# Kernel tuning notes

Measured on AMD Instinct MI355X. Metric: run time of the kernel, lower is better.

Reference implementation:

```python
import jax, jax.numpy as jnp
import numpy as np

N_NODES = 32768
N_EDGES = 524288
HID = 128


def _linear_params(key, fan_in, fan_out):
    kw, kb = jax.random.split(key)
    bound = 1.0 / np.sqrt(fan_in)
    w = jax.random.uniform(kw, (fan_in, fan_out), jnp.float32, -bound, bound)
    b = jax.random.uniform(kb, (fan_out,), jnp.float32, -bound, bound)
    return w, b


def setup_inputs() -> dict:
    key = jax.random.key(0)
    ks = jax.random.split(key, 8)
    x = jax.random.normal(ks[0], (N_NODES, HID), jnp.float32)
    edge_attr = jax.random.normal(ks[1], (N_EDGES, HID), jnp.float32)
    edges = jax.random.randint(ks[2], (2, N_EDGES), 0, N_NODES, jnp.int32)
    w1, b1 = _linear_params(ks[3], 3 * HID, HID)      # message_fn layer 1
    w2, b2 = _linear_params(ks[4], HID, HID)          # message_fn layer 2
    wu1, bu1 = _linear_params(ks[5], HID, 2 * HID)    # update_fn layer 1
    wu2, bu2 = _linear_params(ks[6], 2 * HID, HID)    # update_fn layer 2
    return {"x": x, "edge_attr": edge_attr, "edges": edges,
            "w1": w1, "b1": b1, "w2": w2, "b2": b2,
            "wu1": wu1, "bu1": bu1, "wu2": wu2, "bu2": bu2}


def reference(x, edge_attr, edges, w1, b1, w2, b2, wu1, bu1, wu2, bu2):
    n_nodes = x.shape[0]
    send, recv = edges[0], edges[1]
    # gather endpoint features and concat with edge attributes: [E, 3*HID]
    ea = jnp.concatenate([x[send], x[recv], edge_attr], axis=-1)
    # per-edge message MLP (Linear-SiLU-Linear-SiLU)
    h = jax.nn.silu(ea @ w1 + b1)
    msg = jax.nn.silu(h @ w2 + b2)                    # [E, HID]
    # scatter-mean into receiving nodes
    sums = jax.ops.segment_sum(msg, recv, num_segments=n_nodes)
    counts = jax.ops.segment_sum(jnp.ones((msg.shape[0],), msg.dtype), recv,
                                 num_segments=n_nodes)
    aggr = sums / jnp.maximum(counts, 1.0)[:, None]
    # residual (input_size == hidden_size -> Identity) + update MLP
    xo = x + aggr
    xo = xo + (jax.nn.silu(xo @ wu1 + bu1) @ wu2 + bu2)
    return xo, msg
```

## Files before the change

kernel.cpp:

```cpp
#include <hip/hip_runtime.h>
#include <hip/hip_bf16.h>

#define NN 32768
#define NE 524288
#define HID 128

typedef unsigned short u16;
typedef unsigned int u32;
typedef __bf16 bf16x8 __attribute__((ext_vector_type(8)));
typedef float f32x4 __attribute__((ext_vector_type(4)));

__device__ __forceinline__ u16 f2bf(float f) {
  return __builtin_bit_cast(u16, (__bf16)f);
}
__device__ __forceinline__ float silu_f(float v) {
  return v * __builtin_amdgcn_rcpf(1.f + __expf(-v));
}
__device__ __forceinline__ bf16x8 cvt8(float4 a, float4 b) {
  bf16x8 r;
  r[0] = (__bf16)a.x; r[1] = (__bf16)a.y; r[2] = (__bf16)a.z; r[3] = (__bf16)a.w;
  r[4] = (__bf16)b.x; r[5] = (__bf16)b.y; r[6] = (__bf16)b.z; r[7] = (__bf16)b.w;
  return r;
}
__device__ __forceinline__ float4 f4fma(float4 x, float4 s, float inv) {
  return make_float4(x.x + s.x * inv, x.y + s.y * inv,
                     x.z + s.z * inv, x.w + s.w * inv);
}

__device__ __forceinline__ void gld16(const void* g, void* l) {
  __builtin_amdgcn_global_load_lds(
      (const __attribute__((address_space(1))) u32*)g,
      (__attribute__((address_space(3))) u32*)l, 16, 0, 0);
}

#define WV(N)  do { asm volatile("s_waitcnt vmcnt(" #N ")" ::: "memory"); \
                    __builtin_amdgcn_sched_barrier(0); } while (0)
#define WL()   do { asm volatile("s_waitcnt lgkmcnt(0)" ::: "memory"); \
                    __builtin_amdgcn_sched_barrier(0); } while (0)
__device__ __forceinline__ void bar() {
  __builtin_amdgcn_sched_barrier(0);
  __builtin_amdgcn_s_barrier();
  __builtin_amdgcn_sched_barrier(0);
}

__global__ __launch_bounds__(256) void prep_k(
    const float* __restrict__ x, const float* __restrict__ w1,
    const float* __restrict__ w2, const float* __restrict__ wu1,
    const float* __restrict__ wu2, const int* __restrict__ recv,
    u16* __restrict__ xb, u16* __restrict__ w1Ts, u16* __restrict__ w2Ts,
    u16* __restrict__ wu1T, u16* __restrict__ wu2T, int* __restrict__ cnt)
{
  int i = blockIdx.x * 256 + threadIdx.x;
  xb[i] = f2bf(x[i]);
  if (i < NE) atomicAdd(&cnt[recv[i]], 1);
  if (i < 3 * 128 * 128) {
    int j = i & 7, qs = (i >> 3) & 15, c = (i >> 7) & 127, s = i >> 14;
    int k = s * 128 + ((qs ^ (c & 7)) << 3) + j;
    w1Ts[i] = f2bf(w1[k * 128 + c]);
  }
  if (i < 128 * 128) {
    int j = i & 7, qs = (i >> 3) & 15, c = i >> 7;
    int k = ((qs ^ (c & 7)) << 3) + j;
    w2Ts[i] = f2bf(w2[k * 128 + c]);
  }
  if (i < 256 * 128) { int c = i >> 7, k = i & 127; wu1T[i] = f2bf(wu1[k * 256 + c]); }
  if (i < 128 * 256) { int c = i >> 8, k = i & 255; wu2T[i] = f2bf(wu2[k * 128 + c]); }
}

__global__ __launch_bounds__(1024) void scan_k(const int* __restrict__ cnt,
                                               int* __restrict__ cursor)
{
  __shared__ int part[1024];
  const int tid = threadIdx.x;
  const int base = tid * 32;
  int v[32];
  int s = 0;
  #pragma unroll
  for (int j = 0; j < 32; ++j) { v[j] = cnt[base + j]; s += v[j]; }
  part[tid] = s;
  __syncthreads();
  #pragma unroll 1
  for (int d = 1; d < 1024; d <<= 1) {
    int t = (tid >= d) ? part[tid - d] : 0;
    __syncthreads();
    part[tid] += t;
    __syncthreads();
  }
  int ex = part[tid] - s;
  #pragma unroll
  for (int j = 0; j < 32; ++j) {
    cursor[base + j] = ex;
    ex += v[j];
  }
}

__global__ __launch_bounds__(256) void scatter_k(const int* __restrict__ recv,
                                                 int* __restrict__ cursor,
                                                 int* __restrict__ eperm)
{
  int e = blockIdx.x * 256 + threadIdx.x;
  int r = recv[e];
  int pos = atomicAdd(&cursor[r], 1);
  eperm[pos] = e;
}

__global__ __launch_bounds__(512, 4) void edge_mlp(
    const u16* __restrict__ xb, const float* __restrict__ eattr,
    const int* __restrict__ send, const int* __restrict__ recv,
    const int* __restrict__ eperm,
    const u16* __restrict__ w1Ts, const float* __restrict__ b1,
    const u16* __restrict__ w2Ts, const float* __restrict__ b2,
    float* __restrict__ msg_out, float* __restrict__ sums)
{
  __shared__ u16 sA0[64 * 128];
  __shared__ u16 sA1[64 * 128];
  __shared__ u16 sB[128 * 128 / 2 * 2];
  __shared__ int sNid[64];

  const int tid  = threadIdx.x;
  const int lane = tid & 63;
  const int w    = tid >> 6;
  const int wr   = w >> 2;
  const int wc   = w & 3;
  const int fr   = lane & 15;
  const int fkq  = lane >> 4;
  const int orow = fkq * 4;
  const int lrow4 = lane >> 4;
  const int schk  = lane & 15;
  const int logical = ((int)blockIdx.x & 7) * ((int)gridDim.x >> 3)
                    + ((int)blockIdx.x >> 3);
  const int e0 = logical * 64;

  int eo[2], ns[2], nr[2], rl[2];
  #pragma unroll
  for (int i = 0; i < 2; ++i) {
    rl[i] = w * 8 + i * 4 + lrow4;
    eo[i] = eperm[e0 + rl[i]];
  }
  #pragma unroll
  for (int i = 0; i < 2; ++i) {
    ns[i] = send[eo[i]];
    nr[i] = recv[eo[i]];
    if (schk == 0) sNid[rl[i]] = nr[i];
  }

  f32x4 acc[2][2];
  #pragma unroll
  for (int m = 0; m < 2; ++m)
    #pragma unroll
    for (int n = 0; n < 2; ++n)
      #pragma unroll
      for (int r = 0; r < 4; ++r) acc[m][n][r] = 0.f;

  float b1v[2], b2v[2];
  #pragma unroll
  for (int n = 0; n < 2; ++n) {
    b1v[n] = b1[wc * 32 + n * 16 + fr];
    b2v[n] = b2[wc * 32 + n * 16 + fr];
  }
  __builtin_amdgcn_sched_barrier(0);
  #pragma unroll
  for (int i = 0; i < 2; ++i)
    gld16(xb + ((size_t)ns[i] << 7) + ((schk ^ (rl[i] & 7)) << 3),
          sA0 + ((w * 8 + i * 4) << 7));
  #pragma unroll
  for (int i = 0; i < 4; ++i)
    gld16(w1Ts + ((w * 16 + i * 4) << 7) + (lane << 3),
          sB + ((w * 16 + i * 4) << 7));
  __builtin_amdgcn_sched_barrier(0);
  #pragma unroll
  for (int i = 0; i < 2; ++i)
    gld16(xb + ((size_t)nr[i] << 7) + ((schk ^ (rl[i] & 7)) << 3),
          sA1 + ((w * 8 + i * 4) << 7));
  __builtin_amdgcn_sched_barrier(0);
  float4 ea[2][2];
  #pragma unroll
  for (int i = 0; i < 2; ++i) {
    const float* ep = eattr + ((size_t)eo[i] << 7) + ((schk ^ (rl[i] & 7)) << 3);
    ea[i][0] = *reinterpret_cast<const float4*>(ep);
    ea[i][1] = *reinterpret_cast<const float4*>(ep + 4);
  }
  __builtin_amdgcn_sched_barrier(0);

  auto cslice = [&](const u16* bufA) {
    #pragma unroll
    for (int kk = 0; kk < 4; ++kk) {
      bf16x8 aF[2], bF[2];
      #pragma unroll
      for (int m = 0; m < 2; ++m) {
        int row = wr * 32 + m * 16 + fr;
        int ch = (kk * 4 + fkq) ^ (row & 7);
        aF[m] = __builtin_bit_cast(bf16x8,
            *reinterpret_cast<const uint4*>(bufA + (row << 7) + (ch << 3)));
      }
      #pragma unroll
      for (int n = 0; n < 2; ++n) {
        int c = wc * 32 + n * 16 + fr;
        int ch = (kk * 4 + fkq) ^ (c & 7);
        bF[n] = __builtin_bit_cast(bf16x8,
            *reinterpret_cast<const uint4*>(sB + (c << 7) + (ch << 3)));
      }
      __builtin_amdgcn_s_setprio(1);
      #pragma unroll
      for (int m = 0; m < 2; ++m)
        #pragma unroll
        for (int n = 0; n < 2; ++n)
          acc[m][n] = __builtin_amdgcn_mfma_f32_16x16x32_bf16(aF[m], bF[n], acc[m][n], 0, 0, 0);
      __builtin_amdgcn_s_setprio(0);
    }
  };

  WV(6); bar();
  cslice(sA0);
  bar();
  #pragma unroll
  for (int i = 0; i < 4; ++i)
    gld16(w1Ts + 16384 + ((w * 16 + i * 4) << 7) + (lane << 3),
          sB + ((w * 16 + i * 4) << 7));
  WV(0); bar();
  cslice(sA1);
  bar();
  #pragma unroll
  for (int i = 0; i < 2; ++i)
    *reinterpret_cast<uint4*>(sA0 + (rl[i] << 7) + (schk << 3)) =
        __builtin_bit_cast(uint4, cvt8(ea[i][0], ea[i][1]));
  #pragma unroll
  for (int i = 0; i < 4; ++i)
    gld16(w1Ts + 32768 + ((w * 16 + i * 4) << 7) + (lane << 3),
          sB + ((w * 16 + i * 4) << 7));
  WV(0); WL(); bar();
  cslice(sA0);
  bar();
  #pragma unroll
  for (int i = 0; i < 4; ++i)
    gld16(w2Ts + ((w * 16 + i * 4) << 7) + (lane << 3),
          sB + ((w * 16 + i * 4) << 7));
  #pragma unroll
  for (int m = 0; m < 2; ++m)
    #pragma unroll
    for (int n = 0; n < 2; ++n) {
      int c = wc * 32 + n * 16 + fr;
      #pragma unroll
      for (int r = 0; r < 4; ++r) {
        int row = wr * 32 + m * 16 + orow + r;
        sA1[(row << 7) + (((c >> 3) ^ (row & 7)) << 3) + (c & 7)] =
            f2bf(silu_f(acc[m][n][r] + b1v[n]));
        acc[m][n][r] = 0.f;
      }
    }
  WV(0); WL(); bar();
  int eg[2][4];
  #pragma unroll
  for (int m = 0; m < 2; ++m)
    #pragma unroll
    for (int r = 0; r < 4; ++r)
      eg[m][r] = eperm[e0 + wr * 32 + m * 16 + orow + r];
  cslice(sA1);
  bar();

  #pragma unroll
  for (int m = 0; m < 2; ++m)
    #pragma unroll
    for (int r = 0; r < 4; ++r) {
      int row = wr * 32 + m * 16 + orow + r;
      float* mp = msg_out + ((size_t)eg[m][r] << 7);
      #pragma unroll
      for (int n = 0; n < 2; ++n) {
        int c = wc * 32 + n * 16 + fr;
        float v = silu_f(acc[m][n][r] + b2v[n]);
        mp[c] = v;
        sA0[(row << 7) + (((c >> 3) ^ (row & 7)) << 3) + (c & 7)] = f2bf(v);
      }
    }
  WL(); bar();

  {
    const int col = tid & 127, q = tid >> 7;
    float s = 0.f;
    int cur = sNid[q * 16];
    #pragma unroll 1
    for (int r = 0; r < 16; ++r) {
      int row = q * 16 + r;
      u16 hv = sA0[(row << 7) + (((col >> 3) ^ (row & 7)) << 3) + (col & 7)];
      s += __builtin_bit_cast(float, (u32)hv << 16);
      int nxt = (r < 15) ? sNid[row + 1] : -1;
      if (nxt != cur) {
        atomicAdd(sums + (size_t)cur * HID + col, s);
        s = 0.f;
        cur = nxt;
      }
    }
  }
}

__global__ __launch_bounds__(256) void mlp1_k(
    const float* __restrict__ x, const float* __restrict__ sums,
    const int* __restrict__ cnt, const u16* __restrict__ wu1T,
    const float* __restrict__ bu1, u16* __restrict__ t)
{
  __shared__ u16 sB[256][40];
  const int tid = threadIdx.x, lane = tid & 63, wid = tid >> 6;
  const int wr = wid >> 1, wc = wid & 1;
  const int fr = lane & 15, fkq = lane >> 4, fk = fkq * 8, orow = fkq * 4;
  const int n0 = blockIdx.x * 64;

  float invm[2];
  #pragma unroll
  for (int m = 0; m < 2; ++m)
    invm[m] = __builtin_amdgcn_rcpf(fmaxf((float)cnt[n0 + wr * 32 + m * 16 + fr], 1.f));

  f32x4 acc[2][8];
  #pragma unroll
  for (int m = 0; m < 2; ++m)
    #pragma unroll
    for (int n = 0; n < 8; ++n)
      #pragma unroll
      for (int r = 0; r < 4; ++r) acc[m][n][r] = 0.f;

  #pragma unroll 1
  for (int kk = 0; kk < 4; ++kk) {
    #pragma unroll
    for (int it = 0; it < 4; ++it) {
      int chunk = tid + it * 256;
      int c = chunk >> 2, q = chunk & 3;
      *reinterpret_cast<uint4*>(&sB[c][q * 8]) =
          *reinterpret_cast<const uint4*>(wu1T + c * 128 + kk * 32 + q * 8);
    }
    __syncthreads();
    bf16x8 aF[2], bF[8];
    #pragma unroll
    for (int m = 0; m < 2; ++m) {
      size_t base = (size_t)(n0 + wr * 32 + m * 16 + fr) * HID + kk * 32 + fk;
      float4 xv0 = *reinterpret_cast<const float4*>(x + base);
      float4 xv1 = *reinterpret_cast<const float4*>(x + base + 4);
      float4 sv0 = *reinterpret_cast<const float4*>(sums + base);
      float4 sv1 = *reinterpret_cast<const float4*>(sums + base + 4);
      aF[m] = cvt8(f4fma(xv0, sv0, invm[m]), f4fma(xv1, sv1, invm[m]));
    }
    #pragma unroll
    for (int n = 0; n < 8; ++n)
      bF[n] = __builtin_bit_cast(bf16x8,
          *reinterpret_cast<const uint4*>(&sB[wc * 128 + n * 16 + fr][fk]));
    #pragma unroll
    for (int m = 0; m < 2; ++m)
      #pragma unroll
      for (int n = 0; n < 8; ++n)
        acc[m][n] = __builtin_amdgcn_mfma_f32_16x16x32_bf16(aF[m], bF[n], acc[m][n], 0, 0, 0);
    __syncthreads();
  }
  #pragma unroll
  for (int n = 0; n < 8; ++n) {
    int col = wc * 128 + n * 16 + fr;
    float bb = bu1[col];
    #pragma unroll
    for (int m = 0; m < 2; ++m) {
      int row = n0 + wr * 32 + m * 16 + orow;
      #pragma unroll
      for (int r = 0; r < 4; ++r)
        t[(size_t)(row + r) * 256 + col] = f2bf(silu_f(acc[m][n][r] + bb));
    }
  }
}

__global__ __launch_bounds__(256) void mlp2_k(
    const u16* __restrict__ t, const u16* __restrict__ wu2T,
    const float* __restrict__ bu2, const float* __restrict__ x,
    const float* __restrict__ sums, const int* __restrict__ cnt,
    float* __restrict__ xo)
{
  __shared__ u16 sB[128][40];
  const int tid = threadIdx.x, lane = tid & 63, wid = tid >> 6;
  const int wr = wid >> 1, wc = wid & 1;
  const int fr = lane & 15, fk = (lane >> 4) * 8, orow = (lane >> 4) * 4;
  const int n0 = blockIdx.x * 64;

  f32x4 acc[2][4];
  #pragma unroll
  for (int m = 0; m < 2; ++m)
    #pragma unroll
    for (int n = 0; n < 4; ++n)
      #pragma unroll
      for (int r = 0; r < 4; ++r) acc[m][n][r] = 0.f;

  #pragma unroll 1
  for (int kk = 0; kk < 8; ++kk) {
    #pragma unroll
    for (int it = 0; it < 2; ++it) {
      int chunk = tid + it * 256;
      int c = chunk >> 2, q = chunk & 3;
      *reinterpret_cast<uint4*>(&sB[c][q * 8]) =
          *reinterpret_cast<const uint4*>(wu2T + c * 256 + kk * 32 + q * 8);
    }
    __syncthreads();
    bf16x8 aF[2], bF[4];
    #pragma unroll
    for (int m = 0; m < 2; ++m)
      aF[m] = __builtin_bit_cast(bf16x8, *reinterpret_cast<const uint4*>(
          t + (size_t)(n0 + wr * 32 + m * 16 + fr) * 256 + kk * 32 + fk));
    #pragma unroll
    for (int n = 0; n < 4; ++n)
      bF[n] = __builtin_bit_cast(bf16x8,
          *reinterpret_cast<const uint4*>(&sB[wc * 64 + n * 16 + fr][fk]));
    #pragma unroll
    for (int m = 0; m < 2; ++m)
      #pragma unroll
      for (int n = 0; n < 4; ++n)
        acc[m][n] = __builtin_amdgcn_mfma_f32_16x16x32_bf16(aF[m], bF[n], acc[m][n], 0, 0, 0);
    __syncthreads();
  }
  #pragma unroll
  for (int m = 0; m < 2; ++m) {
    #pragma unroll
    for (int r = 0; r < 4; ++r) {
      int gn = n0 + wr * 32 + m * 16 + orow + r;
      float inv = 1.f / fmaxf((float)cnt[gn], 1.f);
      #pragma unroll
      for (int n = 0; n < 4; ++n) {
        int col = wc * 64 + n * 16 + fr;
        float xi = x[(size_t)gn * HID + col] + sums[(size_t)gn * HID + col] * inv;
        xo[(size_t)gn * HID + col] = xi + acc[m][n][r] + bu2[col];
      }
    }
  }
}

extern "C" void kernel_launch(void* const* d_in, const int* in_sizes, int n_in,
                              void* d_out, int out_size, void* d_ws, size_t ws_size,
                              hipStream_t stream)
{
  (void)in_sizes; (void)n_in; (void)out_size; (void)ws_size;
  const float* x     = (const float*)d_in[0];
  const float* eattr = (const float*)d_in[1];
  const int*   edges = (const int*)d_in[2];
  const float* w1  = (const float*)d_in[3];
  const float* b1  = (const float*)d_in[4];
  const float* w2  = (const float*)d_in[5];
  const float* b2  = (const float*)d_in[6];
  const float* wu1 = (const float*)d_in[7];
  const float* bu1 = (const float*)d_in[8];
  const float* wu2 = (const float*)d_in[9];
  const float* bu2 = (const float*)d_in[10];

  float* xo  = (float*)d_out;
  float* msg = xo + (size_t)NN * HID;

  char* p = (char*)d_ws;
  u16* xb    = (u16*)p; p += (size_t)NN * HID * 2;
  u16* w1Ts  = (u16*)p; p += 384 * 128 * 2;
  u16* w2Ts  = (u16*)p; p += 128 * 128 * 2;
  u16* wu1T  = (u16*)p; p += 256 * 128 * 2;
  u16* wu2T  = (u16*)p; p += 128 * 256 * 2;
  u16* tbuf  = (u16*)p; p += (size_t)NN * 256 * 2;
  float* sums = (float*)p; p += (size_t)NN * HID * 4;
  int* cnt    = (int*)p; p += (size_t)NN * 4;
  int* cursor = (int*)p; p += (size_t)NN * 4;
  int* eperm  = (int*)p; p += (size_t)NE * 4;

  const int* send = edges;
  const int* recv = edges + NE;

  hipMemsetAsync(cnt, 0, (size_t)NN * 4, stream);
  hipMemsetAsync(sums, 0, (size_t)NN * HID * 4, stream);
  prep_k<<<NN * HID / 256, 256, 0, stream>>>(x, w1, w2, wu1, wu2, recv,
                                             xb, w1Ts, w2Ts, wu1T, wu2T, cnt);
  scan_k<<<1, 1024, 0, stream>>>(cnt, cursor);
  scatter_k<<<NE / 256, 256, 0, stream>>>(recv, cursor, eperm);
  edge_mlp<<<NE / 64, 512, 0, stream>>>(xb, eattr, send, recv, eperm,
                                        w1Ts, b1, w2Ts, b2, msg, sums);
  mlp1_k<<<NN / 64, 256, 0, stream>>>(x, sums, cnt, wu1T, bu1, tbuf);
  mlp2_k<<<NN / 64, 256, 0, stream>>>(tbuf, wu2T, bu2, x, sums, cnt, xo);
}
```

Before: 327.1 us.

## Make edge MLP persistent with LDS-resident weights and per-wave edge tiles

Rewrites the edge MLP as a persistent kernel of 256 blocks. Each block loads all layer-1 and layer-2 weights into LDS once, then each wave independently processes eight 32-edge tiles. The wave prefetches the next tile's gathered node features into registers and uses a small per-wave LDS scratch for the hidden activations and the segment reduction. The scatter pass now also writes permuted sender/receiver ids, so the MLP avoids indirect index lookups. This removes repeated weight streaming and block-wide barriers, but keeps only one 512-thread block per CU and puts heavy pressure on registers.

```diff
diff --git a/kernel.cpp b/kernel.cpp
--- a/kernel.cpp
+++ b/kernel.cpp
@@ -12,6 +12,9 @@
 
 __device__ __forceinline__ u16 f2bf(float f) {
   return __builtin_bit_cast(u16, (__bf16)f);
+}
+__device__ __forceinline__ float bf2f(u16 h) {
+  return __builtin_bit_cast(float, (u32)h << 16);
 }
 __device__ __forceinline__ float silu_f(float v) {
   return v * __builtin_amdgcn_rcpf(1.f + __expf(-v));
@@ -33,15 +36,8 @@
       (__attribute__((address_space(3))) u32*)l, 16, 0, 0);
 }
 
-#define WV(N)  do { asm volatile("s_waitcnt vmcnt(" #N ")" ::: "memory"); \
-                    __builtin_amdgcn_sched_barrier(0); } while (0)
 #define WL()   do { asm volatile("s_waitcnt lgkmcnt(0)" ::: "memory"); \
                     __builtin_amdgcn_sched_barrier(0); } while (0)
-__device__ __forceinline__ void bar() {
-  __builtin_amdgcn_sched_barrier(0);
-  __builtin_amdgcn_s_barrier();
-  __builtin_amdgcn_sched_barrier(0);
-}
 
 __global__ __launch_bounds__(256) void prep_k(
     const float* __restrict__ x, const float* __restrict__ w1,
@@ -94,202 +90,223 @@
   }
 }
 
-__global__ __launch_bounds__(256) void scatter_k(const int* __restrict__ recv,
+__global__ __launch_bounds__(256) void scatter_k(const int* __restrict__ send,
+                                                 const int* __restrict__ recv,
                                                  int* __restrict__ cursor,
-                                                 int* __restrict__ eperm)
+                                                 int* __restrict__ eperm,
+                                                 int* __restrict__ sid,
+                                                 int* __restrict__ rid)
 {
   int e = blockIdx.x * 256 + threadIdx.x;
   int r = recv[e];
+  int s = send[e];
   int pos = atomicAdd(&cursor[r], 1);
   eperm[pos] = e;
-}
-
-__global__ __launch_bounds__(512, 4) void edge_mlp(
+  sid[pos] = s;
+  rid[pos] = r;
+}
+
+__global__ __launch_bounds__(512, 2) void edge_mlp(
     const u16* __restrict__ xb, const float* __restrict__ eattr,
-    const int* __restrict__ send, const int* __restrict__ recv,
-    const int* __restrict__ eperm,
-    const u16* __restrict__ w1Ts, const float* __restrict__ b1,
-    const u16* __restrict__ w2Ts, const float* __restrict__ b2,
+    const int* __restrict__ eperm, const int* __restrict__ sid,
+    const int* __restrict__ rid,
+    const u16* __restrict__ wTs, const float* __restrict__ b1,
+    const float* __restrict__ b2,
     float* __restrict__ msg_out, float* __restrict__ sums)
 {
-  __shared__ u16 sA0[64 * 128];
-  __shared__ u16 sA1[64 * 128];
-  __shared__ u16 sB[128 * 128 / 2 * 2];
-  __shared__ int sNid[64];
+  __shared__ u16 sW[65536];
+  __shared__ u16 sT[8][1280];
 
   const int tid  = threadIdx.x;
   const int lane = tid & 63;
   const int w    = tid >> 6;
-  const int wr   = w >> 2;
-  const int wc   = w & 3;
   const int fr   = lane & 15;
   const int fkq  = lane >> 4;
   const int orow = fkq * 4;
-  const int lrow4 = lane >> 4;
-  const int schk  = lane & 15;
-  const int logical = ((int)blockIdx.x & 7) * ((int)gridDim.x >> 3)
-                    + ((int)blockIdx.x >> 3);
-  const int e0 = logical * 64;
-
-  int eo[2], ns[2], nr[2], rl[2];
-  #pragma unroll
-  for (int i = 0; i < 2; ++i) {
-    rl[i] = w * 8 + i * 4 + lrow4;
-    eo[i] = eperm[e0 + rl[i]];
-  }
-  #pragma unroll
-  for (int i = 0; i < 2; ++i) {
-    ns[i] = send[eo[i]];
-    nr[i] = recv[eo[i]];
-    if (schk == 0) sNid[rl[i]] = nr[i];
-  }
-
-  f32x4 acc[2][2];
-  #pragma unroll
-  for (int m = 0; m < 2; ++m)
-    #pragma unroll
-    for (int n = 0; n < 2; ++n)
-      #pragma unroll
-      for (int r = 0; r < 4; ++r) acc[m][n][r] = 0.f;
-
-  float b1v[2], b2v[2];
-  #pragma unroll
-  for (int n = 0; n < 2; ++n) {
-    b1v[n] = b1[wc * 32 + n * 16 + fr];
-    b2v[n] = b2[wc * 32 + n * 16 + fr];
-  }
-  __builtin_amdgcn_sched_barrier(0);
-  #pragma unroll
-  for (int i = 0; i < 2; ++i)
-    gld16(xb + ((size_t)ns[i] << 7) + ((schk ^ (rl[i] & 7)) << 3),
-          sA0 + ((w * 8 + i * 4) << 7));
-  #pragma unroll
-  for (int i = 0; i < 4; ++i)
-    gld16(w1Ts + ((w * 16 + i * 4) << 7) + (lane << 3),
-          sB + ((w * 16 + i * 4) << 7));
-  __builtin_amdgcn_sched_barrier(0);
-  #pragma unroll
-  for (int i = 0; i < 2; ++i)
-    gld16(xb + ((size_t)nr[i] << 7) + ((schk ^ (rl[i] & 7)) << 3),
-          sA1 + ((w * 8 + i * 4) << 7));
-  __builtin_amdgcn_sched_barrier(0);
-  float4 ea[2][2];
-  #pragma unroll
-  for (int i = 0; i < 2; ++i) {
-    const float* ep = eattr + ((size_t)eo[i] << 7) + ((schk ^ (rl[i] & 7)) << 3);
-    ea[i][0] = *reinterpret_cast<const float4*>(ep);
-    ea[i][1] = *reinterpret_cast<const float4*>(ep + 4);
-  }
-  __builtin_amdgcn_sched_barrier(0);
-
-  auto cslice = [&](const u16* bufA) {
+  const int half = lane >> 5;
+  const int cloc = lane & 31;
+
+  #pragma unroll
+  for (int i = 0; i < 16; ++i)
+    gld16(wTs + (size_t)(i * 512 + tid) * 8, sW + (size_t)(i * 512 + w * 64) * 8);
+  asm volatile("s_waitcnt vmcnt(0)" ::: "memory");
+  __builtin_amdgcn_s_barrier();
+
+  float b1v[8], b2v[8];
+  #pragma unroll
+  for (int n = 0; n < 8; ++n) {
+    b1v[n] = b1[n * 16 + fr];
+    b2v[n] = b2[n * 16 + fr];
+  }
+
+  const int xcd = blockIdx.x & 7, jj = blockIdx.x >> 3;
+  int base = (xcd * 2048 + (jj * 8 + w) * 8) * 32;
+
+  int eoA = eperm[base + fr], eoB = eperm[base + 16 + fr];
+  int nsA = sid[base + fr],   nsB = sid[base + 16 + fr];
+  int nrA = rid[base + fr],   nrB = rid[base + 16 + fr];
+
+  bf16x8 a0[4][2], a1[4][2];
+  #pragma unroll
+  for (int kk = 0; kk < 4; ++kk) {
+    a0[kk][0] = *reinterpret_cast<const bf16x8*>(xb + (size_t)nsA * 128 + kk * 32 + fkq * 8);
+    a0[kk][1] = *reinterpret_cast<const bf16x8*>(xb + (size_t)nsB * 128 + kk * 32 + fkq * 8);
+    a1[kk][0] = *reinterpret_cast<const bf16x8*>(xb + (size_t)nrA * 128 + kk * 32 + fkq * 8);
+    a1[kk][1] = *reinterpret_cast<const bf16x8*>(xb + (size_t)nrB * 128 + kk * 32 + fkq * 8);
+  }
+
+  u16* tch = &sT[w][0];
+
+  auto slice = [&](const bf16x8 (&A)[4][2], int P, f32x4 (&C)[2][8]) {
     #pragma unroll
     for (int kk = 0; kk < 4; ++kk) {
-      bf16x8 aF[2], bF[2];
-      #pragma unroll
-      for (int m = 0; m < 2; ++m) {
-        int row = wr * 32 + m * 16 + fr;
-        int ch = (kk * 4 + fkq) ^ (row & 7);
-        aF[m] = __builtin_bit_cast(bf16x8,
-            *reinterpret_cast<const uint4*>(bufA + (row << 7) + (ch << 3)));
-      }
-      #pragma unroll
-      for (int n = 0; n < 2; ++n) {
-        int c = wc * 32 + n * 16 + fr;
+      bf16x8 bF[8];
+      #pragma unroll
+      for (int n = 0; n < 8; ++n) {
+        int c = n * 16 + fr;
         int ch = (kk * 4 + fkq) ^ (c & 7);
         bF[n] = __builtin_bit_cast(bf16x8,
-            *reinterpret_cast<const uint4*>(sB + (c << 7) + (ch << 3)));
+            *reinterpret_cast<const uint4*>(sW + P * 16384 + (c << 7) + (ch << 3)));
       }
       __builtin_amdgcn_s_setprio(1);
       #pragma unroll
       for (int m = 0; m < 2; ++m)
         #pragma unroll
-        for (int n = 0; n < 2; ++n)
-          acc[m][n] = __builtin_amdgcn_mfma_f32_16x16x32_bf16(aF[m], bF[n], acc[m][n], 0, 0, 0);
+        for (int n = 0; n < 8; ++n)
+          C[m][n] = __builtin_amdgcn_mfma_f32_16x16x32_bf16(A[kk][m], bF[n], C[m][n], 0, 0, 0);
       __builtin_amdgcn_s_setprio(0);
     }
   };
 
-  WV(6); bar();
-  cslice(sA0);
-  bar();
-  #pragma unroll
-  for (int i = 0; i < 4; ++i)
-    gld16(w1Ts + 16384 + ((w * 16 + i * 4) << 7) + (lane << 3),
-          sB + ((w * 16 + i * 4) << 7));
-  WV(0); bar();
-  cslice(sA1);
-  bar();
-  #pragma unroll
-  for (int i = 0; i < 2; ++i)
-    *reinterpret_cast<uint4*>(sA0 + (rl[i] << 7) + (schk << 3)) =
-        __builtin_bit_cast(uint4, cvt8(ea[i][0], ea[i][1]));
-  #pragma unroll
-  for (int i = 0; i < 4; ++i)
-    gld16(w1Ts + 32768 + ((w * 16 + i * 4) << 7) + (lane << 3),
-          sB + ((w * 16 + i * 4) << 7));
-  WV(0); WL(); bar();
-  cslice(sA0);
-  bar();
-  #pragma unroll
-  for (int i = 0; i < 4; ++i)
-    gld16(w2Ts + ((w * 16 + i * 4) << 7) + (lane << 3),
-          sB + ((w * 16 + i * 4) << 7));
-  #pragma unroll
-  for (int m = 0; m < 2; ++m)
-    #pragma unroll
-    for (int n = 0; n < 2; ++n) {
-      int c = wc * 32 + n * 16 + fr;
-      #pragma unroll
-      for (int r = 0; r < 4; ++r) {
-        int row = wr * 32 + m * 16 + orow + r;
-        sA1[(row << 7) + (((c >> 3) ^ (row & 7)) << 3) + (c & 7)] =
-            f2bf(silu_f(acc[m][n][r] + b1v[n]));
-        acc[m][n][r] = 0.f;
+  #pragma unroll 1
+  for (int t = 0; t < 8; ++t) {
+    float4 ea[2][8];
+    const float* epA = eattr + ((size_t)eoA << 7) + fkq * 8;
+    const float* epB = eattr + ((size_t)eoB << 7) + fkq * 8;
+    #pragma unroll
+    for (int kk = 0; kk < 4; ++kk) {
+      ea[0][2 * kk]     = *reinterpret_cast<const float4*>(epA + kk * 32);
+      ea[0][2 * kk + 1] = *reinterpret_cast<const float4*>(epA + kk * 32 + 4);
+      ea[1][2 * kk]     = *reinterpret_cast<const float4*>(epB + kk * 32);
+      ea[1][2 * kk + 1] = *reinterpret_cast<const float4*>(epB + kk * 32 + 4);
+    }
+    int eg[2][4];
+    #pragma unroll
+    for (int m = 0; m < 2; ++m)
+      #pragma unroll
+      for (int r = 0; r < 4; ++r)
+        eg[m][r] = eperm[base + m * 16 + orow + r];
+    int nid[16];
+    #pragma unroll
+    for (int r = 0; r < 16; ++r) nid[r] = rid[base + half * 16 + r];
+    int base1 = (t < 7) ? base + 32 : base;
+    int eoA1 = eperm[base1 + fr], eoB1 = eperm[base1 + 16 + fr];
+    int nsA1 = sid[base1 + fr],   nsB1 = sid[base1 + 16 + fr];
+    int nrA1 = rid[base1 + fr],   nrB1 = rid[base1 + 16 + fr];
+    __builtin_amdgcn_sched_barrier(0);
+
+    f32x4 acc[2][8];
+    #pragma unroll
+    for (int m = 0; m < 2; ++m)
+      #pragma unroll
+      for (int n = 0; n < 8; ++n)
+        #pragma unroll
+        for (int r = 0; r < 4; ++r) acc[m][n][r] = 0.f;
+
+    slice(a0, 0, acc);
+    slice(a1, 1, acc);
+    bf16x8 ae[4][2];
+    #pragma unroll
+    for (int kk = 0; kk < 4; ++kk) {
+      ae[kk][0] = cvt8(ea[0][2 * kk], ea[0][2 * kk + 1]);
+      ae[kk][1] = cvt8(ea[1][2 * kk], ea[1][2 * kk + 1]);
+    }
+    slice(ae, 2, acc);
+
+    f32x4 acc2[2][8];
+    #pragma unroll
+    for (int m = 0; m < 2; ++m)
+      #pragma unroll
+      for (int n = 0; n < 8; ++n)
+        #pragma unroll
+        for (int r = 0; r < 4; ++r) acc2[m][n][r] = 0.f;
+
+    #pragma unroll
+    for (int kk = 0; kk < 4; ++kk) {
+      #pragma unroll
+      for (int m = 0; m < 2; ++m)
+        #pragma unroll
+        for (int nl = 0; nl < 2; ++nl) {
+          int n = 2 * kk + nl;
+          #pragma unroll
+          for (int r = 0; r < 4; ++r)
+            tch[(m * 16 + orow + r) * 40 + nl * 16 + fr] =
+                f2bf(silu_f(acc[m][n][r] + b1v[n]));
+        }
+      WL();
+      bf16x8 ah[2];
+      ah[0] = __builtin_bit_cast(bf16x8,
+          *reinterpret_cast<const uint4*>(tch + fr * 40 + fkq * 8));
+      ah[1] = __builtin_bit_cast(bf16x8,
+          *reinterpret_cast<const uint4*>(tch + (16 + fr) * 40 + fkq * 8));
+      bf16x8 bF[8];
+      #pragma unroll
+      for (int n = 0; n < 8; ++n) {
+        int c = n * 16 + fr;
+        int ch = (kk * 4 + fkq) ^ (c & 7);
+        bF[n] = __builtin_bit_cast(bf16x8,
+            *reinterpret_cast<const uint4*>(sW + 3 * 16384 + (c << 7) + (ch << 3)));
       }
-    }
-  WV(0); WL(); bar();
-  int eg[2][4];
-  #pragma unroll
-  for (int m = 0; m < 2; ++m)
-    #pragma unroll
-    for (int r = 0; r < 4; ++r)
-      eg[m][r] = eperm[e0 + wr * 32 + m * 16 + orow + r];
-  cslice(sA1);
-  bar();
-
-  #pragma unroll
-  for (int m = 0; m < 2; ++m)
-    #pragma unroll
-    for (int r = 0; r < 4; ++r) {
-      int row = wr * 32 + m * 16 + orow + r;
-      float* mp = msg_out + ((size_t)eg[m][r] << 7);
-      #pragma unroll
-      for (int n = 0; n < 2; ++n) {
-        int c = wc * 32 + n * 16 + fr;
-        float v = silu_f(acc[m][n][r] + b2v[n]);
-        mp[c] = v;
-        sA0[(row << 7) + (((c >> 3) ^ (row & 7)) << 3) + (c & 7)] = f2bf(v);
+      __builtin_amdgcn_s_setprio(1);
+      #pragma unroll
+      for (int m = 0; m < 2; ++m)
+        #pragma unroll
+        for (int n = 0; n < 8; ++n)
+          acc2[m][n] = __builtin_amdgcn_mfma_f32_16x16x32_bf16(ah[m], bF[n], acc2[m][n], 0, 0, 0);
+      __builtin_amdgcn_s_setprio(0);
+    }
+
+    #pragma unroll
+    for (int kk = 0; kk < 4; ++kk) {
+      a0[kk][0] = *reinterpret_cast<const bf16x8*>(xb + (size_t)nsA1 * 128 + kk * 32 + fkq * 8);
+      a0[kk][1] = *reinterpret_cast<const bf16x8*>(xb + (size_t)nsB1 * 128 + kk * 32 + fkq * 8);
+      a1[kk][0] = *reinterpret_cast<const bf16x8*>(xb + (size_t)nrA1 * 128 + kk * 32 + fkq * 8);
+      a1[kk][1] = *reinterpret_cast<const bf16x8*>(xb + (size_t)nrB1 * 128 + kk * 32 + fkq * 8);
+    }
+    __builtin_amdgcn_sched_barrier(0);
+
+    #pragma unroll
+    for (int cc = 0; cc < 4; ++cc) {
+      #pragma unroll
+      for (int m = 0; m < 2; ++m)
+        #pragma unroll
+        for (int nl = 0; nl < 2; ++nl) {
+          int n = 2 * cc + nl;
+          #pragma unroll
+          for (int r = 0; r < 4; ++r) {
+            float v = silu_f(acc2[m][n][r] + b2v[n]);
+            msg_out[((size_t)eg[m][r] << 7) + n * 16 + fr] = v;
+            tch[(m * 16 + orow + r) * 40 + nl * 16 + fr] = f2bf(v);
+          }
+        }
+      WL();
+      float s = 0.f;
+      int cur = nid[0];
+      #pragma unroll
+      for (int r = 0; r < 16; ++r) {
+        s += bf2f(tch[(half * 16 + r) * 40 + cloc]);
+        int nxt = (r < 15) ? nid[r + 1] : -1;
+        if (nxt != cur) {
+          atomicAdd(sums + (size_t)cur * HID + cc * 32 + cloc, s);
+          s = 0.f;
+          cur = nxt;
+        }
       }
-    }
-  WL(); bar();
-
-  {
-    const int col = tid & 127, q = tid >> 7;
-    float s = 0.f;
-    int cur = sNid[q * 16];
-    #pragma unroll 1
-    for (int r = 0; r < 16; ++r) {
-      int row = q * 16 + r;
-      u16 hv = sA0[(row << 7) + (((col >> 3) ^ (row & 7)) << 3) + (col & 7)];
-      s += __builtin_bit_cast(float, (u32)hv << 16);
-      int nxt = (r < 15) ? sNid[row + 1] : -1;
-      if (nxt != cur) {
-        atomicAdd(sums + (size_t)cur * HID + col, s);
-        s = 0.f;
-        cur = nxt;
-      }
-    }
+      WL();
+    }
+
+    base = base1;
+    eoA = eoA1; eoB = eoB1;
   }
 }
 
@@ -330,11 +347,11 @@
     bf16x8 aF[2], bF[8];
     #pragma unroll
     for (int m = 0; m < 2; ++m) {
-      size_t base = (size_t)(n0 + wr * 32 + m * 16 + fr) * HID + kk * 32 + fk;
-      float4 xv0 = *reinterpret_cast<const float4*>(x + base);
-      float4 xv1 = *reinterpret_cast<const float4*>(x + base + 4);
-      float4 sv0 = *reinterpret_cast<const float4*>(sums + base);
-      float4 sv1 = *reinterpret_cast<const float4*>(sums + base + 4);
+      size_t basei = (size_t)(n0 + wr * 32 + m * 16 + fr) * HID + kk * 32 + fk;
+      float4 xv0 = *reinterpret_cast<const float4*>(x + basei);
+      float4 xv1 = *reinterpret_cast<const float4*>(x + basei + 4);
+      float4 sv0 = *reinterpret_cast<const float4*>(sums + basei);
+      float4 sv1 = *reinterpret_cast<const float4*>(sums + basei + 4);
       aF[m] = cvt8(f4fma(xv0, sv0, invm[m]), f4fma(xv1, sv1, invm[m]));
     }
     #pragma unroll
@@ -455,6 +472,8 @@
   int* cnt    = (int*)p; p += (size_t)NN * 4;
   int* cursor = (int*)p; p += (size_t)NN * 4;
   int* eperm  = (int*)p; p += (size_t)NE * 4;
+  int* sid    = (int*)p; p += (size_t)NE * 4;
+  int* rid    = (int*)p; p += (size_t)NE * 4;
 
   const int* send = edges;
   const int* recv = edges + NE;
@@ -464,9 +483,9 @@
   prep_k<<<NN * HID / 256, 256, 0, stream>>>(x, w1, w2, wu1, wu2, recv,
                                              xb, w1Ts, w2Ts, wu1T, wu2T, cnt);
   scan_k<<<1, 1024, 0, stream>>>(cnt, cursor);
-  scatter_k<<<NE / 256, 256, 0, stream>>>(recv, cursor, eperm);
-  edge_mlp<<<NE / 64, 512, 0, stream>>>(xb, eattr, send, recv, eperm,
-                                        w1Ts, b1, w2Ts, b2, msg, sums);
+  scatter_k<<<NE / 256, 256, 0, stream>>>(send, recv, cursor, eperm, sid, rid);
+  edge_mlp<<<256, 512, 0, stream>>>(xb, eattr, eperm, sid, rid,
+                                    w1Ts, b1, b2, msg, sums);
   mlp1_k<<<NN / 64, 256, 0, stream>>>(x, sums, cnt, wu1T, bu1, tbuf);
   mlp2_k<<<NN / 64, 256, 0, stream>>>(tbuf, wu2T, bu2, x, sums, cnt, xo);
 }
```

Result: faster. 297.1 us (-9.2%).
